# Optimization experiments

Hardware: AMD Instinct MI355X
Metric: run time of the kernel (lower is better)

## Reference

```python
import jax, jax.numpy as jnp
import numpy as np

# Dims per init_kwargs / input_specs
B, L, D = 2, 4096, 512
H = 8            # num_heads -> head_dim = 64
N, P = 32, 64    # num_nodes, partition_length -> N*P = 2048 queries
TEMP = 0.7       # temperature (!= 1.0 -> rescale path active)
LN_EPS = 1e-5


def layernorm(x, w, b):
    mu = jnp.mean(x, axis=-1, keepdims=True)
    var = jnp.mean(jnp.square(x - mu), axis=-1, keepdims=True)
    return (x - mu) / jnp.sqrt(var + LN_EPS) * w + b


def setup_inputs() -> dict:
    key = jax.random.key(0)
    ks = jax.random.split(key, 4)
    x = jax.random.normal(ks[0], (B, L, D), jnp.float32)
    queries = jax.random.normal(ks[1], (N, P, D), jnp.float32)  # nn.Parameter(randn)
    # MHA in-projection slices for Q and K (V/out_proj do not affect the
    # output when temperature != 1.0: out is recomputed as attn @ x_norm).
    wq = jax.random.normal(ks[2], (D, D), jnp.float32) / np.sqrt(D)
    wk = jax.random.normal(ks[3], (D, D), jnp.float32) / np.sqrt(D)
    bq = jnp.zeros((D,), jnp.float32)
    bk = jnp.zeros((D,), jnp.float32)
    gamma_q = jnp.ones((D,), jnp.float32)
    beta_q = jnp.zeros((D,), jnp.float32)
    gamma_x = jnp.ones((D,), jnp.float32)
    beta_x = jnp.zeros((D,), jnp.float32)
    return dict(x=x, queries=queries, wq=wq, wk=wk, bq=bq, bk=bk,
                gamma_q=gamma_q, beta_q=beta_q, gamma_x=gamma_x, beta_x=beta_x)


def reference(x, queries, wq, wk, bq, bk, gamma_q, beta_q, gamma_x, beta_x):
    # q: [B, N*P, D] (expanded learnable query bank), then LayerNorms
    q = jnp.broadcast_to(queries[None], (B, N, P, D)).reshape(B, N * P, D)
    q = layernorm(q, gamma_q, beta_q)
    xn = layernorm(x, gamma_x, beta_x)
    hd = D // H
    # torch MHA scales Q by 1/sqrt(head_dim)
    qp = ((q @ wq.T + bq).reshape(B, N * P, H, hd)) * (1.0 / np.sqrt(hd))
    kp = (xn @ wk.T + bk).reshape(B, L, H, hd)
    scores = jnp.einsum('bqhd,bkhd->bhqk', qp, kp)            # [B,H,NP,L]
    attn = jax.nn.softmax(scores, axis=-1).mean(axis=1)       # head-avg [B,NP,L]
    # temperature-rescaled softmax (temp != 1.0 path)
    attn = jax.nn.softmax((jnp.log(attn) + 1e-9) / TEMP, axis=-1)
    out = jnp.einsum('bql,bld->bqd', attn, xn)                # [B,NP,D]
    return out.reshape(B, N, P, D)
```

## Files before the change

kernel.cpp:

```cpp
#include <hip/hip_runtime.h>
#include <hip/hip_bf16.h>
#include <math.h>

#define Dd   512
#define Hn   8
#define Bn   2
#define Ln   4096
#define NPn  2048
#define INV_T 1.42857142857142857f

typedef __attribute__((ext_vector_type(8))) short short8;
typedef __attribute__((ext_vector_type(4))) float f32x4;

__device__ __forceinline__ ushort bf16_rne(float x) {
    uint u = __builtin_bit_cast(uint, x);
    return (ushort)((u + 0x7fffu + ((u >> 16) & 1u)) >> 16);
}
__device__ __forceinline__ float bf16_tof(ushort h) {
    uint u = ((uint)h) << 16; return __builtin_bit_cast(float, u);
}

__global__ __launch_bounds__(64) void ln_split(
    const float* __restrict__ x, const float* __restrict__ qsrc,
    const float* __restrict__ gx, const float* __restrict__ bx,
    const float* __restrict__ gq, const float* __restrict__ bq,
    ushort* __restrict__ xh, ushort* __restrict__ xl,
    ushort* __restrict__ qnh, ushort* __restrict__ qnl)
{
    int row = blockIdx.x;
    const float* src; ushort* dh; ushort* dl; const float* g; const float* be;
    if (row < Bn * Ln) {
        src = x + (size_t)row * Dd; dh = xh + (size_t)row * Dd; dl = xl + (size_t)row * Dd;
        g = gx; be = bx;
    } else {
        int r = row - Bn * Ln;
        src = qsrc + (size_t)r * Dd; dh = qnh + (size_t)r * Dd; dl = qnl + (size_t)r * Dd;
        g = gq; be = bq;
    }
    int t = threadIdx.x;
    float4 v0 = ((const float4*)src)[2 * t];
    float4 v1 = ((const float4*)src)[2 * t + 1];
    float s = v0.x + v0.y + v0.z + v0.w + v1.x + v1.y + v1.z + v1.w;
#pragma unroll
    for (int o = 32; o > 0; o >>= 1) s += __shfl_down(s, o);
    float mu = __shfl(s, 0) * (1.0f / Dd);
    float a[8] = {v0.x - mu, v0.y - mu, v0.z - mu, v0.w - mu,
                  v1.x - mu, v1.y - mu, v1.z - mu, v1.w - mu};
    float s2 = 0.f;
#pragma unroll
    for (int i = 0; i < 8; ++i) s2 += a[i] * a[i];
#pragma unroll
    for (int o = 32; o > 0; o >>= 1) s2 += __shfl_down(s2, o);
    float rstd = rsqrtf(__shfl(s2, 0) * (1.0f / Dd) + 1e-5f);
    float4 g0 = ((const float4*)g)[2 * t],  g1 = ((const float4*)g)[2 * t + 1];
    float4 b0 = ((const float4*)be)[2 * t], b1 = ((const float4*)be)[2 * t + 1];
    float gv[8] = {g0.x, g0.y, g0.z, g0.w, g1.x, g1.y, g1.z, g1.w};
    float bv[8] = {b0.x, b0.y, b0.z, b0.w, b1.x, b1.y, b1.z, b1.w};
    ushort hv[8], lv[8];
#pragma unroll
    for (int i = 0; i < 8; ++i) {
        float v = a[i] * rstd * gv[i] + bv[i];
        hv[i] = bf16_rne(v);
        lv[i] = bf16_rne(v - bf16_tof(hv[i]));
    }
    *(ushort4*)&dh[t * 8]     = make_ushort4(hv[0], hv[1], hv[2], hv[3]);
    *(ushort4*)&dh[t * 8 + 4] = make_ushort4(hv[4], hv[5], hv[6], hv[7]);
    *(ushort4*)&dl[t * 8]     = make_ushort4(lv[0], lv[1], lv[2], lv[3]);
    *(ushort4*)&dl[t * 8 + 4] = make_ushort4(lv[4], lv[5], lv[6], lv[7]);
}

__global__ __launch_bounds__(256) void wsplit(
    const float* __restrict__ wq, const float* __restrict__ wk,
    ushort* __restrict__ wqh, ushort* __restrict__ wql,
    ushort* __restrict__ wkh, ushort* __restrict__ wkl)
{
    int i = blockIdx.x * 256 + threadIdx.x;
    const float* src; ushort* dh; ushort* dl;
    int j = i;
    if (i < 65536) { src = wq; dh = wqh; dl = wql; }
    else { j -= 65536; src = wk; dh = wkh; dl = wkl; }
    float4 v = ((const float4*)src)[j];
    float vv[4] = {v.x, v.y, v.z, v.w};
    ushort hv[4], lv[4];
#pragma unroll
    for (int k = 0; k < 4; ++k) {
        hv[k] = bf16_rne(vv[k]);
        lv[k] = bf16_rne(vv[k] - bf16_tof(hv[k]));
    }
    *(ushort4*)&dh[j * 4] = make_ushort4(hv[0], hv[1], hv[2], hv[3]);
    *(ushort4*)&dl[j * 4] = make_ushort4(lv[0], lv[1], lv[2], lv[3]);
}

__global__ __launch_bounds__(256, 2) void proj_mfma(
    const ushort* __restrict__ Ah, const ushort* __restrict__ Al,
    const ushort* __restrict__ Wh, const ushort* __restrict__ Wl,
    const float* __restrict__ bias,
    ushort* __restrict__ Chi, ushort* __restrict__ Clo, float scale)
{
    int bm = blockIdx.x * 64, bn = blockIdx.y * 256;
    int t = threadIdx.x, wv = t >> 6, ln = t & 63;
    int lq = ln & 15, lg = ln >> 4;
    f32x4 acc[4][4] = {};
    for (int k0 = 0; k0 < Dd; k0 += 32) {
        short8 bh[4], bl[4];
#pragma unroll
        for (int nf = 0; nf < 4; ++nf) {
            size_t wr = (size_t)(bn + wv * 64 + nf * 16 + lq) * Dd + k0 + lg * 8;
            bh[nf] = *(const short8*)&Wh[wr];
            bl[nf] = *(const short8*)&Wl[wr];
        }
#pragma unroll
        for (int qt = 0; qt < 4; ++qt) {
            size_t ar = (size_t)(bm + qt * 16 + lq) * Dd + k0 + lg * 8;
            short8 ah = *(const short8*)&Ah[ar];
            short8 al = *(const short8*)&Al[ar];
#pragma unroll
            for (int nf = 0; nf < 4; ++nf) {
                acc[qt][nf] = __builtin_amdgcn_mfma_f32_16x16x32_bf16(ah, bh[nf], acc[qt][nf], 0, 0, 0);
                acc[qt][nf] = __builtin_amdgcn_mfma_f32_16x16x32_bf16(ah, bl[nf], acc[qt][nf], 0, 0, 0);
                acc[qt][nf] = __builtin_amdgcn_mfma_f32_16x16x32_bf16(al, bh[nf], acc[qt][nf], 0, 0, 0);
            }
        }
    }
    float bb[4];
#pragma unroll
    for (int nf = 0; nf < 4; ++nf) bb[nf] = bias[bn + wv * 64 + nf * 16 + lq];
#pragma unroll
    for (int qt = 0; qt < 4; ++qt)
#pragma unroll
        for (int nf = 0; nf < 4; ++nf)
#pragma unroll
            for (int r = 0; r < 4; ++r) {
                int m = bm + qt * 16 + lg * 4 + r;
                int n = bn + wv * 64 + nf * 16 + lq;
                float v = scale * (acc[qt][nf][r] + bb[nf]);
                ushort hi = bf16_rne(v);
                Chi[(size_t)m * Dd + n] = hi;
                Clo[(size_t)m * Dd + n] = bf16_rne(v - bf16_tof(hi));
            }
}

__global__ __launch_bounds__(256) void transpose_u16(
    const ushort* __restrict__ xh, const ushort* __restrict__ xl,
    ushort* __restrict__ vh, ushort* __restrict__ vl)
{
    __shared__ uint tile[64][65];
    int l0 = blockIdx.x * 64, d0 = blockIdx.y * 64, b = blockIdx.z;
    int t = threadIdx.x;
#pragma unroll
    for (int i = 0; i < 16; ++i) {
        int idx = i * 256 + t, lr = idx >> 6, lc = idx & 63;
        size_t o = ((size_t)(b * Ln + l0 + lr)) * Dd + d0 + lc;
        tile[lr][lc] = (uint)xh[o] | ((uint)xl[o] << 16);
    }
    __syncthreads();
#pragma unroll
    for (int i = 0; i < 16; ++i) {
        int idx = i * 256 + t, dr = idx >> 6, lc = idx & 63;
        uint v = tile[lc][dr];
        size_t o = ((size_t)(b * Dd + d0 + dr)) * Ln + l0 + lc;
        vh[o] = (ushort)(v & 0xffff);
        vl[o] = (ushort)(v >> 16);
    }
}

#define MFMA6(acc, ah0, ah1, al0, al1, bh0, bh1, bl0, bl1)                         \
    acc = __builtin_amdgcn_mfma_f32_16x16x32_bf16(ah0, bh0, acc, 0, 0, 0);         \
    acc = __builtin_amdgcn_mfma_f32_16x16x32_bf16(ah0, bl0, acc, 0, 0, 0);         \
    acc = __builtin_amdgcn_mfma_f32_16x16x32_bf16(al0, bh0, acc, 0, 0, 0);         \
    acc = __builtin_amdgcn_mfma_f32_16x16x32_bf16(ah1, bh1, acc, 0, 0, 0);         \
    acc = __builtin_amdgcn_mfma_f32_16x16x32_bf16(ah1, bl1, acc, 0, 0, 0);         \
    acc = __builtin_amdgcn_mfma_f32_16x16x32_bf16(al1, bh1, acc, 0, 0, 0);

__global__ __launch_bounds__(256, 4) void attn_pass1(
    const ushort* __restrict__ qh_g, const ushort* __restrict__ ql_g,
    const ushort* __restrict__ kh_g, const ushort* __restrict__ kl_g,
    float* __restrict__ zpart)
{
    int orig = blockIdx.x;
    int combo = orig & 15, b = combo & 1, ck = combo >> 1;
    int q0 = (orig >> 4) * 32;
    int t = threadIdx.x, wv = t >> 6, ln = t & 63;
    int lq = ln & 15, lg = ln >> 4;
    int h0 = wv * 2;

    short8 AH[2][2][2], AL[2][2][2];
#pragma unroll
    for (int qt = 0; qt < 2; ++qt)
#pragma unroll
        for (int hh = 0; hh < 2; ++hh)
#pragma unroll
            for (int hf = 0; hf < 2; ++hf) {
                size_t a = (size_t)(q0 + qt * 16 + lq) * Dd + (h0 + hh) * 64 + hf * 32 + lg * 8;
                AH[qt][hh][hf] = *(const short8*)&qh_g[a];
                AL[qt][hh][hf] = *(const short8*)&ql_g[a];
            }

    float z[2][2][4] = {};
    size_t krow = ((size_t)(b * Ln + ck * 512 + lq)) * Dd + lg * 8;
    for (int step = 0; step < 32; ++step) {
        size_t kstep = krow + (size_t)step * 16 * Dd;
#pragma unroll
        for (int hh = 0; hh < 2; ++hh) {
            const short* kR = (const short*)kh_g + kstep + (h0 + hh) * 64;
            const short* lR = (const short*)kl_g + kstep + (h0 + hh) * 64;
            short8 bh0 = *(const short8*)&kR[0],  bh1 = *(const short8*)&kR[32];
            short8 bl0 = *(const short8*)&lR[0],  bl1 = *(const short8*)&lR[32];
#pragma unroll
            for (int qt = 0; qt < 2; ++qt) {
                f32x4 acc = {};
                MFMA6(acc, AH[qt][hh][0], AH[qt][hh][1], AL[qt][hh][0], AL[qt][hh][1],
                      bh0, bh1, bl0, bl1);
#pragma unroll
                for (int r = 0; r < 4; ++r) z[hh][qt][r] += __expf(acc[r]);
            }
        }
    }
#pragma unroll
    for (int hh = 0; hh < 2; ++hh)
#pragma unroll
        for (int qt = 0; qt < 2; ++qt)
#pragma unroll
            for (int r = 0; r < 4; ++r) {
                float v = z[hh][qt][r];
                v += __shfl_xor(v, 1); v += __shfl_xor(v, 2);
                v += __shfl_xor(v, 4); v += __shfl_xor(v, 8);
                z[hh][qt][r] = v;
            }
    if (lq == 0) {
#pragma unroll
        for (int hh = 0; hh < 2; ++hh)
#pragma unroll
            for (int qt = 0; qt < 2; ++qt)
#pragma unroll
                for (int r = 0; r < 4; ++r) {
                    int q = q0 + qt * 16 + lg * 4 + r;
                    zpart[((size_t)(ck * 2 + b) * NPn + q) * 8 + h0 + hh] = z[hh][qt][r];
                }
    }
}

__global__ __launch_bounds__(256) void zreduce(
    const float* __restrict__ zpart, float* __restrict__ izs)
{
    int g = blockIdx.x * 256 + threadIdx.x;
    int b = g >> 14, q = (g >> 3) & 2047, h = g & 7;
    float s = 0.f;
#pragma unroll
    for (int c = 0; c < 8; ++c)
        s += zpart[((size_t)(c * 2 + b) * NPn + q) * 8 + h];
    izs[g] = 1.0f / (8.0f * s);
}

__global__ __launch_bounds__(512, 4) void attn_pass2(
    const ushort* __restrict__ qh_g, const ushort* __restrict__ ql_g,
    const ushort* __restrict__ kh_g, const ushort* __restrict__ kl_g,
    const ushort* __restrict__ vh_g, const ushort* __restrict__ vl_g,
    const float* __restrict__ izs,
    float* __restrict__ Opart, float* __restrict__ rpart)
{
    __shared__ __align__(16) short8 qhs[2048];
    __shared__ __align__(16) short8 qls[2048];
    __shared__ __align__(16) ushort Ps[32 * 128];
    __shared__ float izss[256];
    __shared__ float rss[8][32];

    int orig = blockIdx.x;
    int combo = orig & 7, b = combo & 1, ck = combo >> 1;
    int q0 = (orig >> 3) * 32;
    int t = threadIdx.x, wv = t >> 6, ln = t & 63;
    int lq = ln & 15, lg = ln >> 4;
    const short8* qh8 = (const short8*)qh_g;
    const short8* ql8 = (const short8*)ql_g;
    const short8* Ps8 = (const short8*)Ps;

#pragma unroll
    for (int it = 0; it < 4; ++it) {
        int idx = it * 512 + t; int r = idx >> 6;
        int slot = idx ^ (r & 7);
        qhs[slot] = qh8[(size_t)(q0 + r) * 64 + (idx & 63)];
        qls[slot] = ql8[(size_t)(q0 + r) * 64 + (idx & 63)];
    }
    if (t < 256) izss[t] = izs[((size_t)b * NPn + q0 + (t >> 3)) * 8 + (t & 7)];
    __syncthreads();

    f32x4 oacc[2][4] = {};
    float racc[2][4] = {};

    for (int g = 0; g < 4; ++g) {
        int t0 = ck * 1024 + g * 256;
        float p[2][2][4] = {};
        size_t krow = ((size_t)(b * Ln + t0 + wv * 16 + lq)) * Dd + lg * 8;
#pragma unroll
        for (int h = 0; h < 8; ++h) {
            short8 ah0[2], ah1[2], al0[2], al1[2];
#pragma unroll
            for (int qt = 0; qt < 2; ++qt) {
                int row = qt * 16 + lq;
                int base = row * 64 + h * 8;
                int sw = row & 7;
                ah0[qt] = qhs[(base + lg) ^ sw];
                ah1[qt] = qhs[(base + 4 + lg) ^ sw];
                al0[qt] = qls[(base + lg) ^ sw];
                al1[qt] = qls[(base + 4 + lg) ^ sw];
            }
#pragma unroll
            for (int kt = 0; kt < 2; ++kt) {
                const short* kR = (const short*)kh_g + krow + (size_t)kt * 128 * Dd + h * 64;
                const short* lR = (const short*)kl_g + krow + (size_t)kt * 128 * Dd + h * 64;
                short8 bh0 = *(const short8*)&kR[0],  bh1 = *(const short8*)&kR[32];
                short8 bl0 = *(const short8*)&lR[0],  bl1 = *(const short8*)&lR[32];
#pragma unroll
                for (int qt = 0; qt < 2; ++qt) {
                    f32x4 acc = {};
                    MFMA6(acc, ah0[qt], ah1[qt], al0[qt], al1[qt], bh0, bh1, bl0, bl1);
#pragma unroll
                    for (int r = 0; r < 4; ++r)
                        p[kt][qt][r] += __expf(acc[r]) * izss[(qt * 16 + lg * 4 + r) * 8 + h];
                }
            }
        }
#pragma unroll
        for (int kt = 0; kt < 2; ++kt) {
#pragma unroll
            for (int qt = 0; qt < 2; ++qt)
#pragma unroll
                for (int r = 0; r < 4; ++r) {
                    int q = qt * 16 + lg * 4 + r;
                    float wgt = __expf(INV_T * __logf(p[kt][qt][r]));
                    ushort uw = bf16_rne(wgt);
                    racc[qt][r] += bf16_tof(uw);
                    int e = q * 128 + wv * 16 + lq;
                    Ps[e ^ ((q & 7) << 3)] = uw;
                }
            __syncthreads();
            short8 pa[2][4];
#pragma unroll
            for (int qt = 0; qt < 2; ++qt)
#pragma unroll
                for (int ks = 0; ks < 4; ++ks) {
                    int row = qt * 16 + lq;
                    pa[qt][ks] = Ps8[(row * 16 + ks * 4 + lg) ^ (row & 7)];
                }
#pragma unroll
            for (int n = 0; n < 4; ++n) {
                size_t vrow = ((size_t)(b * Dd + wv * 64 + n * 16 + lq)) * Ln
                              + t0 + kt * 128 + lg * 8;
                const short* vR = (const short*)vh_g + vrow;
                const short* wR = (const short*)vl_g + vrow;
#pragma unroll
                for (int ks = 0; ks < 4; ++ks) {
                    short8 bh = *(const short8*)&vR[ks * 32];
                    short8 bl = *(const short8*)&wR[ks * 32];
#pragma unroll
                    for (int qt = 0; qt < 2; ++qt) {
                        oacc[qt][n] = __builtin_amdgcn_mfma_f32_16x16x32_bf16(pa[qt][ks], bh, oacc[qt][n], 0, 0, 0);
                        oacc[qt][n] = __builtin_amdgcn_mfma_f32_16x16x32_bf16(pa[qt][ks], bl, oacc[qt][n], 0, 0, 0);
                    }
                }
            }
            __syncthreads();
        }
    }

#pragma unroll
    for (int qt = 0; qt < 2; ++qt)
#pragma unroll
        for (int r = 0; r < 4; ++r) {
            float v = racc[qt][r];
            v += __shfl_xor(v, 1); v += __shfl_xor(v, 2);
            v += __shfl_xor(v, 4); v += __shfl_xor(v, 8);
            racc[qt][r] = v;
        }
    if (lq == 0) {
#pragma unroll
        for (int qt = 0; qt < 2; ++qt)
#pragma unroll
            for (int r = 0; r < 4; ++r) rss[wv][qt * 16 + lg * 4 + r] = racc[qt][r];
    }
    __syncthreads();
    if (t < 32) {
        float s = 0.f;
#pragma unroll
        for (int w2 = 0; w2 < 8; ++w2) s += rss[w2][t];
        rpart[(size_t)(ck * 2 + b) * NPn + q0 + t] = s;
    }
#pragma unroll
    for (int qt = 0; qt < 2; ++qt)
#pragma unroll
        for (int n = 0; n < 4; ++n)
#pragma unroll
            for (int r = 0; r < 4; ++r) {
                int q = q0 + qt * 16 + lg * 4 + r;
                int d = wv * 64 + n * 16 + lq;
                Opart[((size_t)(ck * 2 + b) * NPn + q) * Dd + d] = oacc[qt][n][r];
            }
}

__global__ __launch_bounds__(256) void finalize(
    const float* __restrict__ Opart, const float* __restrict__ rpart,
    float* __restrict__ out)
{
    int idx = blockIdx.x * 256 + threadIdx.x;
    int d4 = idx & 127, q = (idx >> 7) & 2047, b = idx >> 18;
    float rs = 0.f;
#pragma unroll
    for (int c = 0; c < 4; ++c) rs += rpart[(size_t)(c * 2 + b) * NPn + q];
    float ox = 0.f, oy = 0.f, oz = 0.f, ow = 0.f;
#pragma unroll
    for (int c = 0; c < 4; ++c) {
        float4 v = ((const float4*)Opart)[((size_t)(c * 2 + b) * NPn + q) * 128 + d4];
        ox += v.x; oy += v.y; oz += v.z; ow += v.w;
    }
    float inv = 1.0f / rs;
    ((float4*)out)[idx] = make_float4(ox * inv, oy * inv, oz * inv, ow * inv);
}

extern "C" void kernel_launch(void* const* d_in, const int* in_sizes, int n_in,
                              void* d_out, int out_size, void* d_ws, size_t ws_size,
                              hipStream_t stream)
{
    (void)in_sizes; (void)n_in; (void)out_size; (void)ws_size;
    const float* x       = (const float*)d_in[0];
    const float* queries = (const float*)d_in[1];
    const float* wq      = (const float*)d_in[2];
    const float* wk      = (const float*)d_in[3];
    const float* bq      = (const float*)d_in[4];
    const float* bk      = (const float*)d_in[5];
    const float* gq      = (const float*)d_in[6];
    const float* betq    = (const float*)d_in[7];
    const float* gx      = (const float*)d_in[8];
    const float* betx    = (const float*)d_in[9];

    const size_t XN = (size_t)Bn * Ln * Dd;
    const size_t QN = (size_t)NPn * Dd;
    const size_t WN = (size_t)Dd * Dd;

    ushort* u = (ushort*)d_ws;
    ushort* xh  = u;             ushort* xl  = xh + XN;
    ushort* qnh = xl + XN;       ushort* qnl = qnh + QN;
    ushort* wqh = qnl + QN;      ushort* wql = wqh + WN;
    ushort* wkh = wql + WN;      ushort* wkl = wkh + WN;
    ushort* kh  = wkl + WN;      ushort* kl  = kh + XN;
    ushort* qh  = kl + XN;       ushort* ql  = qh + QN;
    ushort* vh  = ql + QN;       ushort* vl  = vh + XN;
    float* f = (float*)(vl + XN);
    float* zpart = f;
    float* izs   = zpart + 262144;
    float* rpart = izs + 32768;
    float* Opart = rpart + 16384;

    ln_split<<<Bn * Ln + NPn, 64, 0, stream>>>(x, queries, gx, betx, gq, betq,
                                               xh, xl, qnh, qnl);
    wsplit<<<512, 256, 0, stream>>>(wq, wk, wqh, wql, wkh, wkl);
    proj_mfma<<<dim3((Bn * Ln) / 64, 2), 256, 0, stream>>>(xh, xl, wkh, wkl, bk, kh, kl, 1.0f);
    proj_mfma<<<dim3(NPn / 64, 2), 256, 0, stream>>>(qnh, qnl, wqh, wql, bq, qh, ql, 0.125f);
    transpose_u16<<<dim3(Ln / 64, Dd / 64, Bn), 256, 0, stream>>>(xh, xl, vh, vl);
    attn_pass1<<<1024, 256, 0, stream>>>(qh, ql, kh, kl, zpart);
    zreduce<<<128, 256, 0, stream>>>(zpart, izs);
    attn_pass2<<<512, 512, 0, stream>>>(qh, ql, kh, kl, vh, vl, izs, Opart, rpart);
    finalize<<<2048, 256, 0, stream>>>(Opart, rpart, (float*)d_out);
}
```

Measured before the change: 545.2 us.

## Split pass1 by head group, software-pipeline K loads, add nontemporal memory hints

attn_pass1 now gives each wave one head instead of two and doubles the grid, which shrinks register use and raises parallelism. In both attention passes the K fragment loads are double-buffered so the next step's global loads are issued before the current MFMAs. attn_pass2 loops heads inside each key tile, reloads Q fragments from LDS per head, and hoists the V loads ahead of its MFMA chain. Nontemporal loads and stores are added for Q, Opart and finalize; the risk is more redundant Q loading and higher register pressure from the prefetched buffers.

```diff
diff --git a/kernel.cpp b/kernel.cpp
--- a/kernel.cpp
+++ b/kernel.cpp
@@ -178,65 +178,70 @@
     float* __restrict__ zpart)
 {
     int orig = blockIdx.x;
-    int combo = orig & 15, b = combo & 1, ck = combo >> 1;
-    int q0 = (orig >> 4) * 32;
+    int combo = orig & 31, b = combo & 1, ck = (combo >> 1) & 7, hg = combo >> 4;
+    int q0 = (orig >> 5) * 32;
     int t = threadIdx.x, wv = t >> 6, ln = t & 63;
     int lq = ln & 15, lg = ln >> 4;
-    int h0 = wv * 2;
-
-    short8 AH[2][2][2], AL[2][2][2];
+    int h = hg * 4 + wv;
+
+    short8 AH[2][2], AL[2][2];
 #pragma unroll
     for (int qt = 0; qt < 2; ++qt)
 #pragma unroll
-        for (int hh = 0; hh < 2; ++hh)
-#pragma unroll
-            for (int hf = 0; hf < 2; ++hf) {
-                size_t a = (size_t)(q0 + qt * 16 + lq) * Dd + (h0 + hh) * 64 + hf * 32 + lg * 8;
-                AH[qt][hh][hf] = *(const short8*)&qh_g[a];
-                AL[qt][hh][hf] = *(const short8*)&ql_g[a];
-            }
-
-    float z[2][2][4] = {};
-    size_t krow = ((size_t)(b * Ln + ck * 512 + lq)) * Dd + lg * 8;
-    for (int step = 0; step < 32; ++step) {
-        size_t kstep = krow + (size_t)step * 16 * Dd;
-#pragma unroll
-        for (int hh = 0; hh < 2; ++hh) {
-            const short* kR = (const short*)kh_g + kstep + (h0 + hh) * 64;
-            const short* lR = (const short*)kl_g + kstep + (h0 + hh) * 64;
-            short8 bh0 = *(const short8*)&kR[0],  bh1 = *(const short8*)&kR[32];
-            short8 bl0 = *(const short8*)&lR[0],  bl1 = *(const short8*)&lR[32];
-#pragma unroll
-            for (int qt = 0; qt < 2; ++qt) {
-                f32x4 acc = {};
-                MFMA6(acc, AH[qt][hh][0], AH[qt][hh][1], AL[qt][hh][0], AL[qt][hh][1],
-                      bh0, bh1, bl0, bl1);
-#pragma unroll
-                for (int r = 0; r < 4; ++r) z[hh][qt][r] += __expf(acc[r]);
-            }
+        for (int hf = 0; hf < 2; ++hf) {
+            size_t a = (size_t)(q0 + qt * 16 + lq) * Dd + h * 64 + hf * 32 + lg * 8;
+            AH[qt][hf] = __builtin_nontemporal_load((const short8*)&qh_g[a]);
+            AL[qt][hf] = __builtin_nontemporal_load((const short8*)&ql_g[a]);
         }
-    }
-#pragma unroll
-    for (int hh = 0; hh < 2; ++hh)
+
+    float z[2][4] = {};
+    const short* kh_p = (const short*)kh_g + ((size_t)(b * Ln + ck * 512 + lq)) * Dd + h * 64 + lg * 8;
+    const short* kl_p = (const short*)kl_g + ((size_t)(b * Ln + ck * 512 + lq)) * Dd + h * 64 + lg * 8;
+
+#define LOADK1(B0, B1, B2, B3, s)                                                  \
+    B0 = *(const short8*)&kh_p[(size_t)(s) * 16 * Dd];                             \
+    B1 = *(const short8*)&kh_p[(size_t)(s) * 16 * Dd + 32];                        \
+    B2 = *(const short8*)&kl_p[(size_t)(s) * 16 * Dd];                             \
+    B3 = *(const short8*)&kl_p[(size_t)(s) * 16 * Dd + 32];
+
+#define STEP1(B0, B1, B2, B3)                                                      \
+    {                                                                              \
+        f32x4 acc0 = {}, acc1 = {};                                                \
+        MFMA6(acc0, AH[0][0], AH[0][1], AL[0][0], AL[0][1], B0, B1, B2, B3);       \
+        MFMA6(acc1, AH[1][0], AH[1][1], AL[1][0], AL[1][1], B0, B1, B2, B3);       \
+        _Pragma("unroll")                                                          \
+        for (int r = 0; r < 4; ++r) {                                              \
+            z[0][r] += __expf(acc0[r]);                                            \
+            z[1][r] += __expf(acc1[r]);                                            \
+        }                                                                          \
+    }
+
+    short8 A0, A1, A2, A3, B0, B1, B2, B3;
+    LOADK1(A0, A1, A2, A3, 0);
+    for (int s = 0; s < 32; s += 2) {
+        LOADK1(B0, B1, B2, B3, s + 1);
+        STEP1(A0, A1, A2, A3);
+        if (s + 2 < 32) { LOADK1(A0, A1, A2, A3, s + 2); }
+        STEP1(B0, B1, B2, B3);
+    }
+
+#pragma unroll
+    for (int qt = 0; qt < 2; ++qt)
+#pragma unroll
+        for (int r = 0; r < 4; ++r) {
+            float v = z[qt][r];
+            v += __shfl_xor(v, 1); v += __shfl_xor(v, 2);
+            v += __shfl_xor(v, 4); v += __shfl_xor(v, 8);
+            z[qt][r] = v;
+        }
+    if (lq == 0) {
 #pragma unroll
         for (int qt = 0; qt < 2; ++qt)
 #pragma unroll
             for (int r = 0; r < 4; ++r) {
-                float v = z[hh][qt][r];
-                v += __shfl_xor(v, 1); v += __shfl_xor(v, 2);
-                v += __shfl_xor(v, 4); v += __shfl_xor(v, 8);
-                z[hh][qt][r] = v;
-            }
-    if (lq == 0) {
-#pragma unroll
-        for (int hh = 0; hh < 2; ++hh)
-#pragma unroll
-            for (int qt = 0; qt < 2; ++qt)
-#pragma unroll
-                for (int r = 0; r < 4; ++r) {
-                    int q = q0 + qt * 16 + lg * 4 + r;
-                    zpart[((size_t)(ck * 2 + b) * NPn + q) * 8 + h0 + hh] = z[hh][qt][r];
-                }
+                int q = q0 + qt * 16 + lg * 4 + r;
+                zpart[((size_t)(ck * 2 + b) * NPn + q) * 8 + h] = z[qt][r];
+            }
     }
 }
 
@@ -278,8 +283,8 @@
     for (int it = 0; it < 4; ++it) {
         int idx = it * 512 + t; int r = idx >> 6;
         int slot = idx ^ (r & 7);
-        qhs[slot] = qh8[(size_t)(q0 + r) * 64 + (idx & 63)];
-        qls[slot] = ql8[(size_t)(q0 + r) * 64 + (idx & 63)];
+        qhs[slot] = __builtin_nontemporal_load(&qh8[(size_t)(q0 + r) * 64 + (idx & 63)]);
+        qls[slot] = __builtin_nontemporal_load(&ql8[(size_t)(q0 + r) * 64 + (idx & 63)]);
     }
     if (t < 256) izss[t] = izs[((size_t)b * NPn + q0 + (t >> 3)) * 8 + (t & 7)];
     __syncthreads();
@@ -287,52 +292,78 @@
     f32x4 oacc[2][4] = {};
     float racc[2][4] = {};
 
+#define QK_H(acc0, acc1, B0, B1, B2, B3, hh)                                       \
+    {                                                                              \
+        int bse = lq * 64 + (hh) * 8;                                              \
+        int sw = lq & 7;                                                           \
+        short8 a0h0 = qhs[(bse + lg) ^ sw];                                        \
+        short8 a0h1 = qhs[(bse + 4 + lg) ^ sw];                                    \
+        short8 a0l0 = qls[(bse + lg) ^ sw];                                        \
+        short8 a0l1 = qls[(bse + 4 + lg) ^ sw];                                    \
+        short8 a1h0 = qhs[(bse + 1024 + lg) ^ sw];                                 \
+        short8 a1h1 = qhs[(bse + 1024 + 4 + lg) ^ sw];                             \
+        short8 a1l0 = qls[(bse + 1024 + lg) ^ sw];                                 \
+        short8 a1l1 = qls[(bse + 1024 + 4 + lg) ^ sw];                             \
+        MFMA6(acc0, a0h0, a0h1, a0l0, a0l1, B0, B1, B2, B3);                       \
+        MFMA6(acc1, a1h0, a1h1, a1l0, a1l1, B0, B1, B2, B3);                       \
+    }
+
+#define LOADK2(B0, B1, B2, B3, hh)                                                 \
+    B0 = *(const short8*)&kRh[(hh) * 64];                                          \
+    B1 = *(const short8*)&kRh[(hh) * 64 + 32];                                     \
+    B2 = *(const short8*)&kRl[(hh) * 64];                                          \
+    B3 = *(const short8*)&kRl[(hh) * 64 + 32];
+
     for (int g = 0; g < 4; ++g) {
         int t0 = ck * 1024 + g * 256;
-        float p[2][2][4] = {};
         size_t krow = ((size_t)(b * Ln + t0 + wv * 16 + lq)) * Dd + lg * 8;
 #pragma unroll
-        for (int h = 0; h < 8; ++h) {
-            short8 ah0[2], ah1[2], al0[2], al1[2];
-#pragma unroll
-            for (int qt = 0; qt < 2; ++qt) {
-                int row = qt * 16 + lq;
-                int base = row * 64 + h * 8;
-                int sw = row & 7;
-                ah0[qt] = qhs[(base + lg) ^ sw];
-                ah1[qt] = qhs[(base + 4 + lg) ^ sw];
-                al0[qt] = qls[(base + lg) ^ sw];
-                al1[qt] = qls[(base + 4 + lg) ^ sw];
-            }
-#pragma unroll
-            for (int kt = 0; kt < 2; ++kt) {
-                const short* kR = (const short*)kh_g + krow + (size_t)kt * 128 * Dd + h * 64;
-                const short* lR = (const short*)kl_g + krow + (size_t)kt * 128 * Dd + h * 64;
-                short8 bh0 = *(const short8*)&kR[0],  bh1 = *(const short8*)&kR[32];
-                short8 bl0 = *(const short8*)&lR[0],  bl1 = *(const short8*)&lR[32];
-#pragma unroll
-                for (int qt = 0; qt < 2; ++qt) {
-                    f32x4 acc = {};
-                    MFMA6(acc, ah0[qt], ah1[qt], al0[qt], al1[qt], bh0, bh1, bl0, bl1);
-#pragma unroll
-                    for (int r = 0; r < 4; ++r)
-                        p[kt][qt][r] += __expf(acc[r]) * izss[(qt * 16 + lg * 4 + r) * 8 + h];
+        for (int kt = 0; kt < 2; ++kt) {
+            const short* kRh = (const short*)kh_g + krow + (size_t)kt * 128 * Dd;
+            const short* kRl = (const short*)kl_g + krow + (size_t)kt * 128 * Dd;
+            float p0[4] = {}, p1[4] = {};
+            short8 A0, A1, A2, A3, B0, B1, B2, B3;
+            LOADK2(A0, A1, A2, A3, 0);
+#pragma unroll
+            for (int h = 0; h < 8; h += 2) {
+                LOADK2(B0, B1, B2, B3, h + 1);
+                {
+                    f32x4 acc0 = {}, acc1 = {};
+                    QK_H(acc0, acc1, A0, A1, A2, A3, h);
+#pragma unroll
+                    for (int r = 0; r < 4; ++r) {
+                        p0[r] += __expf(acc0[r]) * izss[(lg * 4 + r) * 8 + h];
+                        p1[r] += __expf(acc1[r]) * izss[(16 + lg * 4 + r) * 8 + h];
+                    }
                 }
-            }
-        }
-#pragma unroll
-        for (int kt = 0; kt < 2; ++kt) {
-#pragma unroll
-            for (int qt = 0; qt < 2; ++qt)
-#pragma unroll
-                for (int r = 0; r < 4; ++r) {
-                    int q = qt * 16 + lg * 4 + r;
-                    float wgt = __expf(INV_T * __logf(p[kt][qt][r]));
+                if (h + 2 < 8) { LOADK2(A0, A1, A2, A3, h + 2); }
+                {
+                    f32x4 acc0 = {}, acc1 = {};
+                    QK_H(acc0, acc1, B0, B1, B2, B3, h + 1);
+#pragma unroll
+                    for (int r = 0; r < 4; ++r) {
+                        p0[r] += __expf(acc0[r]) * izss[(lg * 4 + r) * 8 + h + 1];
+                        p1[r] += __expf(acc1[r]) * izss[(16 + lg * 4 + r) * 8 + h + 1];
+                    }
+                }
+            }
+#pragma unroll
+            for (int r = 0; r < 4; ++r) {
+                {
+                    int q = lg * 4 + r;
+                    float wgt = __expf(INV_T * __logf(p0[r]));
                     ushort uw = bf16_rne(wgt);
-                    racc[qt][r] += bf16_tof(uw);
-                    int e = q * 128 + wv * 16 + lq;
-                    Ps[e ^ ((q & 7) << 3)] = uw;
+                    racc[0][r] += bf16_tof(uw);
+                    Ps[(q * 128 + wv * 16 + lq) ^ ((q & 7) << 3)] = uw;
                 }
+                {
+                    int q = 16 + lg * 4 + r;
+                    float wgt = __expf(INV_T * __logf(p1[r]));
+                    ushort uw = bf16_rne(wgt);
+                    racc[1][r] += bf16_tof(uw);
+                    Ps[(q * 128 + wv * 16 + lq) ^ ((q & 7) << 3)] = uw;
+                }
+            }
             __syncthreads();
             short8 pa[2][4];
 #pragma unroll
@@ -348,15 +379,20 @@
                               + t0 + kt * 128 + lg * 8;
                 const short* vR = (const short*)vh_g + vrow;
                 const short* wR = (const short*)vl_g + vrow;
-#pragma unroll
-                for (int ks = 0; ks < 4; ++ks) {
-                    short8 bh = *(const short8*)&vR[ks * 32];
-                    short8 bl = *(const short8*)&wR[ks * 32];
-#pragma unroll
-                    for (int qt = 0; qt < 2; ++qt) {
-                        oacc[qt][n] = __builtin_amdgcn_mfma_f32_16x16x32_bf16(pa[qt][ks], bh, oacc[qt][n], 0, 0, 0);
-                        oacc[qt][n] = __builtin_amdgcn_mfma_f32_16x16x32_bf16(pa[qt][ks], bl, oacc[qt][n], 0, 0, 0);
-                    }
+                short8 v0 = *(const short8*)&vR[0],  v1 = *(const short8*)&vR[32];
+                short8 v2 = *(const short8*)&vR[64], v3 = *(const short8*)&vR[96];
+                short8 w0 = *(const short8*)&wR[0],  w1 = *(const short8*)&wR[32];
+                short8 w2 = *(const short8*)&wR[64], w3 = *(const short8*)&wR[96];
+#pragma unroll
+                for (int qt = 0; qt < 2; ++qt) {
+                    oacc[qt][n] = __builtin_amdgcn_mfma_f32_16x16x32_bf16(pa[qt][0], v0, oacc[qt][n], 0, 0, 0);
+                    oacc[qt][n] = __builtin_amdgcn_mfma_f32_16x16x32_bf16(pa[qt][0], w0, oacc[qt][n], 0, 0, 0);
+                    oacc[qt][n] = __builtin_amdgcn_mfma_f32_16x16x32_bf16(pa[qt][1], v1, oacc[qt][n], 0, 0, 0);
+                    oacc[qt][n] = __builtin_amdgcn_mfma_f32_16x16x32_bf16(pa[qt][1], w1, oacc[qt][n], 0, 0, 0);
+                    oacc[qt][n] = __builtin_amdgcn_mfma_f32_16x16x32_bf16(pa[qt][2], v2, oacc[qt][n], 0, 0, 0);
+                    oacc[qt][n] = __builtin_amdgcn_mfma_f32_16x16x32_bf16(pa[qt][2], w2, oacc[qt][n], 0, 0, 0);
+                    oacc[qt][n] = __builtin_amdgcn_mfma_f32_16x16x32_bf16(pa[qt][3], v3, oacc[qt][n], 0, 0, 0);
+                    oacc[qt][n] = __builtin_amdgcn_mfma_f32_16x16x32_bf16(pa[qt][3], w3, oacc[qt][n], 0, 0, 0);
                 }
             }
             __syncthreads();
@@ -393,7 +429,8 @@
             for (int r = 0; r < 4; ++r) {
                 int q = q0 + qt * 16 + lg * 4 + r;
                 int d = wv * 64 + n * 16 + lq;
-                Opart[((size_t)(ck * 2 + b) * NPn + q) * Dd + d] = oacc[qt][n][r];
+                __builtin_nontemporal_store(oacc[qt][n][r],
+                    &Opart[((size_t)(ck * 2 + b) * NPn + q) * Dd + d]);
             }
 }
 
@@ -406,14 +443,15 @@
     float rs = 0.f;
 #pragma unroll
     for (int c = 0; c < 4; ++c) rs += rpart[(size_t)(c * 2 + b) * NPn + q];
-    float ox = 0.f, oy = 0.f, oz = 0.f, ow = 0.f;
+    f32x4 o = {};
 #pragma unroll
     for (int c = 0; c < 4; ++c) {
-        float4 v = ((const float4*)Opart)[((size_t)(c * 2 + b) * NPn + q) * 128 + d4];
-        ox += v.x; oy += v.y; oz += v.z; ow += v.w;
+        f32x4 v = __builtin_nontemporal_load(
+            (const f32x4*)Opart + ((size_t)(c * 2 + b) * NPn + q) * 128 + d4);
+        o += v;
     }
     float inv = 1.0f / rs;
-    ((float4*)out)[idx] = make_float4(ox * inv, oy * inv, oz * inv, ow * inv);
+    ((f32x4*)out)[idx] = o * inv;
 }
 
 extern "C" void kernel_launch(void* const* d_in, const int* in_sizes, int n_in,
@@ -456,7 +494,7 @@
     proj_mfma<<<dim3((Bn * Ln) / 64, 2), 256, 0, stream>>>(xh, xl, wkh, wkl, bk, kh, kl, 1.0f);
     proj_mfma<<<dim3(NPn / 64, 2), 256, 0, stream>>>(qnh, qnl, wqh, wql, bq, qh, ql, 0.125f);
     transpose_u16<<<dim3(Ln / 64, Dd / 64, Bn), 256, 0, stream>>>(xh, xl, vh, vl);
-    attn_pass1<<<1024, 256, 0, stream>>>(qh, ql, kh, kl, zpart);
+    attn_pass1<<<2048, 256, 0, stream>>>(qh, ql, kh, kl, zpart);
     zreduce<<<128, 256, 0, stream>>>(zpart, izs);
     attn_pass2<<<512, 512, 0, stream>>>(qh, ql, kh, kl, vh, vl, izs, Opart, rpart);
     finalize<<<2048, 256, 0, stream>>>(Opart, rpart, (float*)d_out);
```

Measured after the change: 619.5 us. +13.6%, slower.
